# Kernel tuning notes

Hardware: AMD Instinct MI355X
Metric: run time of the kernel (lower is better)

## Reference

```python
import jax, jax.numpy as jnp
import numpy as np

B, T, D = 2, 2048, 2048
H, KV, HD = 16, 8, 128
N_REP = H // KV
EPS = 1e-6
ROPE_THETA = 5e6
K_MASK = float(jnp.finfo(jnp.bfloat16).min)


def setup_inputs() -> dict:
    key = jax.random.key(0)
    ks = jax.random.split(key, 8)
    x = jax.random.normal(ks[0], (B, T, D), dtype=jnp.float32)
    wq = jax.random.normal(ks[1], (D, H * HD), dtype=jnp.float32) * 0.02
    wk = jax.random.normal(ks[2], (D, KV * HD), dtype=jnp.float32) * 0.02
    wv = jax.random.normal(ks[3], (D, KV * HD), dtype=jnp.float32) * 0.02
    wo = jax.random.normal(ks[4], (H * HD, D), dtype=jnp.float32) * 0.02
    qn_w = jnp.ones((HD,), dtype=jnp.float32)
    kn_w = jnp.ones((HD,), dtype=jnp.float32)
    # real rotary angles: [T, HD//2] -> broadcast to [B, T, HD//2]
    pos = jnp.arange(T, dtype=jnp.float32)
    inv_freq = 1.0 / (ROPE_THETA ** (jnp.arange(0, HD, 2, dtype=jnp.float32) / HD))
    ang = pos[:, None] * inv_freq[None, :]
    sin = jnp.broadcast_to(jnp.sin(ang)[None], (B, T, HD // 2))
    cos = jnp.broadcast_to(jnp.cos(ang)[None], (B, T, HD // 2))
    # causal mask [B, 1, T, T]
    causal = jnp.tril(jnp.ones((T, T), dtype=jnp.bool_))
    mask = jnp.broadcast_to(causal[None, None], (B, 1, T, T))
    k_cache = jnp.zeros((B, T, KV, HD), dtype=jnp.float32)
    v_cache = jnp.zeros((B, T, KV, HD), dtype=jnp.float32)
    return {"x": x, "wq": wq, "wk": wk, "wv": wv, "wo": wo,
            "qn_w": qn_w, "kn_w": kn_w, "sin": sin, "cos": cos,
            "mask": mask, "k_cache": k_cache, "v_cache": v_cache}


def _rms_norm(h, w):
    h32 = h.astype(jnp.float32)
    rms = jax.lax.rsqrt(jnp.mean(h32 * h32, axis=-1, keepdims=True) + EPS)
    return (h32 * rms * w).astype(h.dtype)


def _apply_rope(x, sin, cos):
    x1, x2 = x[..., : HD // 2], x[..., HD // 2:]
    s, c = sin[:, :, None, :], cos[:, :, None, :]  # [B,T,1,HD/2]
    return jnp.concatenate([x1 * c - x2 * s, x2 * c + x1 * s], axis=-1).astype(x.dtype)


def reference(x, wq, wk, wv, wo, qn_w, kn_w, sin, cos, mask, k_cache, v_cache):
    b, t, _ = x.shape
    q = _rms_norm((x @ wq).reshape(b, t, H, HD), qn_w)
    k = _rms_norm((x @ wk).reshape(b, t, KV, HD), kn_w)
    v = (x @ wv).reshape(b, t, KV, HD)
    q = _apply_rope(q, sin, cos)
    k = _apply_rope(k, sin, cos)
    # KV-cache update at cur_ind = 0 (prefill)
    k_cache = jax.lax.dynamic_update_slice(k_cache, k.astype(k_cache.dtype), (0, 0, 0, 0))
    v_cache = jax.lax.dynamic_update_slice(v_cache, v.astype(v_cache.dtype), (0, 0, 0, 0))
    # GQA repeat_kv: [B,S,KV,HD] -> [B,S,H,HD]
    kf = jnp.repeat(k_cache, N_REP, axis=2)
    vf = jnp.repeat(v_cache, N_REP, axis=2)
    scale = HD ** -0.5
    # [B,H,T,S]
    attn = jnp.einsum('bthd,bshd->bhts', q, kf) * scale
    attn = jnp.where(mask, attn, K_MASK)
    attn = jax.nn.softmax(attn.astype(jnp.float32), axis=-1).astype(q.dtype)
    out = jnp.einsum('bhts,bshd->bthd', attn, vf).reshape(b, t, H * HD)
    return out @ wo
```

## Files before the change

### kernel.cpp

```cpp
#include <hip/hip_runtime.h>
#include <hip/hip_bf16.h>
#include <stdint.h>

#define BB 2
#define TT 2048
#define DD 2048
#define HH 16
#define KVH 8
#define HDIM 128
#define BT (BB*TT)
#define NQKV (HH*HDIM + 2*KVH*HDIM)
#define TQ (TT/128)
#define ATT_SCALE 0.08838834764831845f
#define RMS_EPS 1e-6f

typedef __bf16 bf16;
typedef __bf16 bf16x8 __attribute__((ext_vector_type(8)));
typedef __bf16 bf16x4 __attribute__((ext_vector_type(4)));
typedef float  f32x4  __attribute__((ext_vector_type(4)));

__device__ __forceinline__ void gl_lds16(const void* g, const void* l) {
  __builtin_amdgcn_global_load_lds(
      (const __attribute__((address_space(1))) void*)(uintptr_t)g,
      (__attribute__((address_space(3))) void*)(uint32_t)(uintptr_t)l,
      16, 0, 0);
}

__global__ __launch_bounds__(256) void cast_bf16_k(const float* __restrict__ in,
                                                   bf16* __restrict__ out, int n4) {
  int i = blockIdx.x * blockDim.x + threadIdx.x;
  int stride = gridDim.x * blockDim.x;
  for (; i < n4; i += stride) {
    float4 v = ((const float4*)in)[i];
    bf16x4 o = { (bf16)v.x, (bf16)v.y, (bf16)v.z, (bf16)v.w };
    *(bf16x4*)(out + (size_t)i * 4) = o;
  }
}

__global__ __launch_bounds__(256) void transpose_cast_k(const float* __restrict__ in,
                                                        bf16* __restrict__ out,
                                                        int R, int C) {
  __shared__ float tile[32][33];
  int tx = threadIdx.x & 31, ty = threadIdx.x >> 5;
  int c0 = blockIdx.x * 32, r0 = blockIdx.y * 32;
#pragma unroll
  for (int i = 0; i < 4; ++i)
    tile[ty + 8*i][tx] = in[(size_t)(r0 + ty + 8*i) * C + c0 + tx];
  __syncthreads();
#pragma unroll
  for (int i = 0; i < 4; ++i)
    out[(size_t)(c0 + ty + 8*i) * R + r0 + tx] = (bf16)tile[tx][ty + 8*i];
}

__global__ __launch_bounds__(256) void transpose_v_k(const bf16* __restrict__ vb,
                                                     bf16* __restrict__ vbt) {
  __shared__ bf16 tile[32][33];
  int tx = threadIdx.x & 31, ty = threadIdx.x >> 5;
  int t0 = blockIdx.x * 32;
  int d0 = blockIdx.y * 32;
  int bk = blockIdx.z;
  int b = bk >> 3, kv = bk & 7;
#pragma unroll
  for (int i = 0; i < 4; ++i)
    tile[ty + 8*i][tx] = vb[(((size_t)(b*TT + t0 + ty + 8*i)) * KVH + kv) * HDIM + d0 + tx];
  __syncthreads();
#pragma unroll
  for (int i = 0; i < 4; ++i)
    vbt[(((size_t)bk) * HDIM + d0 + ty + 8*i) * TT + t0 + tx] = tile[tx][ty + 8*i];
}

template <int OUT_F32>
__global__ __launch_bounds__(512, 2)
void gemm256_k(const bf16* __restrict__ A, const bf16* __restrict__ Bt,
               void* __restrict__ Cout, int M, int N, int K) {
  __shared__ bf16 S[2 * 2 * 2 * 128 * 64];
  const int tid = threadIdx.x, lane = tid & 63, wid = tid >> 6;
  const int lr = lane & 15, lq = lane >> 4;
  const int wrow = wid >> 1, wcol = wid & 1;

  const int nwg = gridDim.x;
  const int o = blockIdx.x;
  const int ns = (o & 7) * (nwg >> 3) + (o >> 3);
  const int GX = N >> 8;
  const int by = ns / GX, bx = ns % GX;

  const int NT = K >> 6;
  const bf16* Ab = A + (size_t)(by * 256) * K;
  const bf16* Bb = Bt + (size_t)(bx * 256) * K;

  const int srow = tid >> 3;
  const size_t soff = (size_t)srow * K + (((tid & 7) ^ (srow & 7)) * 8);
  const int ldst0 = wid * 512;

  auto STAGE = [&](int op, int h, int t_) {
    int tc = t_ < NT ? t_ : NT - 1;
    const bf16* src = (op ? Bb : Ab) + soff + (size_t)(h * 128) * K + tc * 64;
    bf16* dst = S + ((((((t_ & 1) << 1) | op) << 1) | h) << 13) + ldst0;
#pragma unroll
    for (int i = 0; i < 2; ++i)
      gl_lds16(src + (size_t)(i * 64) * K, dst + i * 4096);
  };

  bf16x8 af[2][2][2];
  bf16x8 bfr[4][2];
  f32x4 acc[4][2][4] = {};

  auto LOAD_A = [&](int buf) {
#pragma unroll
    for (int mh = 0; mh < 2; ++mh) {
      const bf16* base = S + (((buf << 2) | mh) << 13);
#pragma unroll
      for (int m = 0; m < 2; ++m) {
        int ra = wrow * 32 + m * 16 + lr;
#pragma unroll
        for (int ks = 0; ks < 2; ++ks)
          af[mh][m][ks] = *(const bf16x8*)(base + ra * 64 + (((ks * 4 + lq) ^ (ra & 7)) * 8));
      }
    }
  };
  auto LOAD_B = [&](int buf, int nh) {
    const bf16* base = S + (((buf << 2) | 2 | nh) << 13);
#pragma unroll
    for (int n = 0; n < 4; ++n) {
      int rb = wcol * 64 + n * 16 + lr;
#pragma unroll
      for (int ks = 0; ks < 2; ++ks)
        bfr[n][ks] = *(const bf16x8*)(base + rb * 64 + (((ks * 4 + lq) ^ (rb & 7)) * 8));
    }
  };
  auto MFMA_Q = [&](int qd, int mh) {
#pragma unroll
    for (int m = 0; m < 2; ++m)
#pragma unroll
      for (int n = 0; n < 4; ++n)
#pragma unroll
        for (int ks = 0; ks < 2; ++ks)
          acc[qd][m][n] = __builtin_amdgcn_mfma_f32_16x16x32_bf16(
              af[mh][m][ks], bfr[n][ks], acc[qd][m][n], 0, 0, 0);
  };

  STAGE(0, 0, 0); STAGE(0, 1, 0); STAGE(1, 0, 0); STAGE(1, 1, 0);
  STAGE(0, 0, 1); STAGE(0, 1, 1); STAGE(1, 0, 1);
  asm volatile("s_waitcnt vmcnt(6)" ::: "memory");
  __builtin_amdgcn_sched_barrier(0);
  __builtin_amdgcn_s_barrier();

  for (int t = 0; t < NT; ++t) {
    const int buf = t & 1;
    LOAD_A(buf);
    LOAD_B(buf, 0);
    STAGE(1, 1, t + 1);
    __builtin_amdgcn_s_barrier();
    asm volatile("s_waitcnt lgkmcnt(0)" ::: "memory");
    __builtin_amdgcn_sched_barrier(0);
    __builtin_amdgcn_s_setprio(1);
    MFMA_Q(0, 0);
    __builtin_amdgcn_s_setprio(0);
    __builtin_amdgcn_sched_barrier(0);
    __builtin_amdgcn_s_barrier();
    STAGE(0, 0, t + 2);
    __builtin_amdgcn_s_barrier();
    __builtin_amdgcn_s_setprio(1);
    MFMA_Q(1, 1);
    __builtin_amdgcn_s_setprio(0);
    __builtin_amdgcn_sched_barrier(0);
    __builtin_amdgcn_s_barrier();
    LOAD_B(buf, 1);
    STAGE(0, 1, t + 2);
    __builtin_amdgcn_s_barrier();
    asm volatile("s_waitcnt lgkmcnt(0)" ::: "memory");
    __builtin_amdgcn_sched_barrier(0);
    __builtin_amdgcn_s_setprio(1);
    MFMA_Q(2, 1);
    __builtin_amdgcn_s_setprio(0);
    __builtin_amdgcn_sched_barrier(0);
    __builtin_amdgcn_s_barrier();
    STAGE(1, 0, t + 2);
    asm volatile("s_waitcnt vmcnt(6)" ::: "memory");
    __builtin_amdgcn_sched_barrier(0);
    __builtin_amdgcn_s_barrier();
    __builtin_amdgcn_s_setprio(1);
    MFMA_Q(3, 0);
    __builtin_amdgcn_s_setprio(0);
    __builtin_amdgcn_sched_barrier(0);
    __builtin_amdgcn_s_barrier();
  }

#pragma unroll
  for (int qd = 0; qd < 4; ++qd) {
    const int mh = (qd == 1 || qd == 2) ? 1 : 0;
    const int nh = (qd >= 2) ? 1 : 0;
#pragma unroll
    for (int m = 0; m < 2; ++m)
#pragma unroll
      for (int n = 0; n < 4; ++n)
#pragma unroll
        for (int j = 0; j < 4; ++j) {
          int row = by * 256 + mh * 128 + wrow * 32 + m * 16 + lq * 4 + j;
          int col = bx * 256 + nh * 128 + wcol * 64 + n * 16 + lr;
          if (OUT_F32) ((float*)Cout)[(size_t)row * N + col] = acc[qd][m][n][j];
          else         ((bf16*)Cout)[(size_t)row * N + col] = (bf16)acc[qd][m][n][j];
        }
  }
}

__global__ __launch_bounds__(256) void norm_rope_k(const bf16* __restrict__ qkv,
                                                   const float* __restrict__ qn_w,
                                                   const float* __restrict__ kn_w,
                                                   const float* __restrict__ sinb,
                                                   const float* __restrict__ cosb,
                                                   bf16* __restrict__ qro,
                                                   bf16* __restrict__ kro,
                                                   bf16* __restrict__ vo) {
  const int bt = blockIdx.x;
  const int tid = threadIdx.x, lane = tid & 63, wid = tid >> 6;
  const bf16* row = qkv + (size_t)bt * NQKV;
  const float sv = sinb[bt * 64 + lane];
  const float cv = cosb[bt * 64 + lane];
  for (int it = 0; it < 8; ++it) {
    int hv = it * 4 + wid;
    int off = (hv < 16) ? hv * 128 : (hv < 24) ? 2048 + (hv - 16) * 128 : 3072 + (hv - 24) * 128;
    float e0 = (float)row[off + lane];
    float e1 = (float)row[off + 64 + lane];
    if (hv >= 24) {
      bf16* dst = vo + (size_t)bt * (KVH * HDIM) + (hv - 24) * 128;
      dst[lane] = (bf16)e0;
      dst[64 + lane] = (bf16)e1;
    } else {
      float ss = e0 * e0 + e1 * e1;
#pragma unroll
      for (int o = 32; o >= 1; o >>= 1) ss += __shfl_xor(ss, o, 64);
      float rms = rsqrtf(ss * (1.0f / 128.0f) + RMS_EPS);
      const float* wn = (hv < 16) ? qn_w : kn_w;
      float n0 = e0 * rms * wn[lane];
      float n1 = e1 * rms * wn[lane + 64];
      float o0 = n0 * cv - n1 * sv;
      float o1 = n1 * cv + n0 * sv;
      if (hv < 16) {
        bf16* dst = qro + (size_t)bt * (HH * HDIM) + hv * 128;
        dst[lane] = (bf16)o0; dst[64 + lane] = (bf16)o1;
      } else {
        bf16* dst = kro + (size_t)bt * (KVH * HDIM) + (hv - 16) * 128;
        dst[lane] = (bf16)o0; dst[64 + lane] = (bf16)o1;
      }
    }
  }
}

__global__ __launch_bounds__(512, 4)
void attn4_k(const bf16* __restrict__ qr, const bf16* __restrict__ kr,
             const bf16* __restrict__ vbt, bf16* __restrict__ ao) {
  __shared__ bf16 Ks[2][64 * 128];
  __shared__ bf16 Vs[2][128 * 64];
  __shared__ bf16 Ps[8 * 16 * 64];
  const int tid = threadIdx.x, lane = tid & 63, wid = tid >> 6;
  const int lr = lane & 15, lq = lane >> 4;
  const int h = blockIdx.y, b = blockIdx.z;
  const int qt = (b & 1) ? (TQ - 1 - blockIdx.x) : blockIdx.x;
  const int kvh = h >> 1;
  const int q0 = qt * 128 + wid * 16;
  const int nt = 2 * qt + 2;

  const int krow0 = lane >> 4, kcc = lane & 15;
  const int vrow0 = lane >> 3, vcc = lane & 7;

  auto STAGE = [&](int bufi, int kt) {
#pragma unroll
    for (int i = 0; i < 2; ++i) {
      int chunk = i * 8 + wid;
      int krow = chunk * 4 + krow0;
      gl_lds16(&kr[(((size_t)(b * TT + kt * 64 + krow)) * KVH + kvh) * HDIM + ((kcc ^ (krow & 7)) * 8)],
               &Ks[bufi][chunk * 512]);
      int drow = chunk * 8 + vrow0;
      gl_lds16(&vbt[(((size_t)(b * KVH + kvh)) * HDIM + drow) * TT + kt * 64 + ((vcc ^ (drow & 7)) * 8)],
               &Vs[bufi][chunk * 512]);
    }
  };

  bf16x8 aq[4];
#pragma unroll
  for (int kk = 0; kk < 4; ++kk)
    aq[kk] = *(const bf16x8*)&qr[(((size_t)(b * TT + q0 + lr)) * HH + h) * HDIM + kk * 32 + lq * 8];

  bf16x8 vones;
#pragma unroll
  for (int j = 0; j < 8; ++j) vones[j] = (bf16)1.0f;

  f32x4 accO[8] = {};
  f32x4 acc1 = {};
  float mrun[4];
#pragma unroll
  for (int r = 0; r < 4; ++r) mrun[r] = -INFINITY;

  int buf = 0;
  STAGE(0, 0);
  __syncthreads();

  for (int kt = 0; kt < nt; ++kt) {
    if (kt + 1 < nt) STAGE(buf ^ 1, kt + 1);

    if (kt * 64 <= q0 + 15) {
      f32x4 sacc[4];
#pragma unroll
      for (int ct = 0; ct < 4; ++ct) {
        sacc[ct] = (f32x4){0.f, 0.f, 0.f, 0.f};
        int krow = ct * 16 + lr;
#pragma unroll
        for (int kk = 0; kk < 4; ++kk) {
          bf16x8 bk = *(const bf16x8*)((const char*)&Ks[buf][0] + krow * 256 + (((kk * 4 + lq) ^ (krow & 7)) * 16));
          sacc[ct] = __builtin_amdgcn_mfma_f32_16x16x32_bf16(aq[kk], bk, sacc[ct], 0, 0, 0);
        }
      }

      const bool domask = (kt * 64 + 63 > q0);
      float p[4][4];
      float pm[4] = {-INFINITY, -INFINITY, -INFINITY, -INFINITY};
#pragma unroll
      for (int ct = 0; ct < 4; ++ct) {
        int col = kt * 64 + ct * 16 + lr;
#pragma unroll
        for (int r = 0; r < 4; ++r) {
          int rowg = q0 + lq * 4 + r;
          float s = (!domask || col <= rowg) ? sacc[ct][r] * ATT_SCALE : -INFINITY;
          p[ct][r] = s;
          pm[r] = fmaxf(pm[r], s);
        }
      }
#pragma unroll
      for (int r = 0; r < 4; ++r) {
#pragma unroll
        for (int o = 1; o < 16; o <<= 1) pm[r] = fmaxf(pm[r], __shfl_xor(pm[r], o, 64));
      }

      int needup = (pm[0] > mrun[0] + 8.f) || (pm[1] > mrun[1] + 8.f) ||
                   (pm[2] > mrun[2] + 8.f) || (pm[3] > mrun[3] + 8.f);
      if (__any(needup)) {
        float alpha[4];
#pragma unroll
        for (int r = 0; r < 4; ++r) {
          float mnew = fmaxf(mrun[r], pm[r]);
          alpha[r] = __expf(mrun[r] - mnew);
          mrun[r] = mnew;
        }
#pragma unroll
        for (int n = 0; n < 8; ++n)
#pragma unroll
          for (int r = 0; r < 4; ++r) accO[n][r] *= alpha[r];
#pragma unroll
        for (int r = 0; r < 4; ++r) acc1[r] *= alpha[r];
      }

#pragma unroll
      for (int ct = 0; ct < 4; ++ct)
#pragma unroll
        for (int r = 0; r < 4; ++r) {
          float e = __expf(p[ct][r] - mrun[r]);
          int prow = lq * 4 + r;
          int col = ct * 16 + lr;
          int cc = col >> 3;
          char* pb = (char*)Ps + (wid * 16 + prow) * 128 + ((cc ^ (prow & 7)) * 16) + (col & 7) * 2;
          *(bf16*)pb = (bf16)e;
        }

#pragma unroll
      for (int c = 0; c < 2; ++c) {
        bf16x8 ap = *(const bf16x8*)((const char*)Ps + (wid * 16 + lr) * 128 + (((c * 4 + lq) ^ (lr & 7)) * 16));
        acc1 = __builtin_amdgcn_mfma_f32_16x16x32_bf16(ap, vones, acc1, 0, 0, 0);
#pragma unroll
        for (int n = 0; n < 8; ++n) {
          int drow = n * 16 + lr;
          bf16x8 bv = *(const bf16x8*)((const char*)&Vs[buf][0] + drow * 128 + (((c * 4 + lq) ^ (drow & 7)) * 16));
          accO[n] = __builtin_amdgcn_mfma_f32_16x16x32_bf16(ap, bv, accO[n], 0, 0, 0);
        }
      }
    }

    __syncthreads();
    buf ^= 1;
  }

  float inv[4];
#pragma unroll
  for (int r = 0; r < 4; ++r) inv[r] = 1.0f / acc1[r];
#pragma unroll
  for (int n = 0; n < 8; ++n)
#pragma unroll
    for (int r = 0; r < 4; ++r) {
      size_t idx = (((size_t)(b * TT + q0 + lq * 4 + r)) * HH + h) * HDIM + n * 16 + lr;
      ao[idx] = (bf16)(accO[n][r] * inv[r]);
    }
}

extern "C" void kernel_launch(void* const* d_in, const int* in_sizes, int n_in,
                              void* d_out, int out_size, void* d_ws, size_t ws_size,
                              hipStream_t stream) {
  const float* x    = (const float*)d_in[0];
  const float* wq   = (const float*)d_in[1];
  const float* wk   = (const float*)d_in[2];
  const float* wv   = (const float*)d_in[3];
  const float* wo   = (const float*)d_in[4];
  const float* qn_w = (const float*)d_in[5];
  const float* kn_w = (const float*)d_in[6];
  const float* sinb = (const float*)d_in[7];
  const float* cosb = (const float*)d_in[8];
  float* out = (float*)d_out;

  char* ws = (char*)d_ws;
  size_t off = 0;
  auto alloc = [&](size_t bytes) {
    char* p = ws + off;
    off += (bytes + 255) & ~(size_t)255;
    return p;
  };
  bf16* xb  = (bf16*)alloc((size_t)BT * DD * 2);
  bf16* Wt  = (bf16*)alloc((size_t)NQKV * DD * 2);
  bf16* Wot = (bf16*)alloc((size_t)DD * DD * 2);
  bf16* qkv = (bf16*)alloc((size_t)BT * NQKV * 2);
  bf16* kro = (bf16*)alloc((size_t)BT * KVH * HDIM * 2);
  bf16* vb  = (bf16*)alloc((size_t)BT * KVH * HDIM * 2);
  bf16* vbt = (bf16*)alloc((size_t)BT * KVH * HDIM * 2);
  bf16* qro = Wt;
  bf16* aob = xb;
  (void)ws_size; (void)in_sizes; (void)n_in; (void)out_size;

  cast_bf16_k<<<2048, 256, 0, stream>>>(x, xb, BT * DD / 4);
  transpose_cast_k<<<dim3(2048 / 32, 2048 / 32), 256, 0, stream>>>(wq, Wt, 2048, 2048);
  transpose_cast_k<<<dim3(1024 / 32, 2048 / 32), 256, 0, stream>>>(wk, Wt + (size_t)2048 * 2048, 2048, 1024);
  transpose_cast_k<<<dim3(1024 / 32, 2048 / 32), 256, 0, stream>>>(wv, Wt + (size_t)3072 * 2048, 2048, 1024);
  transpose_cast_k<<<dim3(2048 / 32, 2048 / 32), 256, 0, stream>>>(wo, Wot, 2048, 2048);

  gemm256_k<0><<<dim3((BT / 256) * (NQKV / 256)), 512, 0, stream>>>(xb, Wt, qkv, BT, NQKV, DD);

  norm_rope_k<<<BT, 256, 0, stream>>>(qkv, qn_w, kn_w, sinb, cosb, qro, kro, vb);
  transpose_v_k<<<dim3(TT / 32, HDIM / 32, BB * KVH), 256, 0, stream>>>(vb, vbt);

  attn4_k<<<dim3(TQ, HH, BB), 512, 0, stream>>>(qro, kro, vbt, aob);

  gemm256_k<1><<<dim3((BT / 256) * (DD / 256)), 512, 0, stream>>>(aob, Wot, out, BT, DD, DD);
}
```

Before: 244.0 us.

## Rewrite attention kernel with 32x32x16 MFMA and register-resident P transposed scores

Replaces the 16x16x32 MFMA attention with a 4-wave block where each wave handles 32 query rows using 32x32x16 bf16 MFMA, computing S transposed (K as A operand) so each lane owns one query column. The probability tile is repacked in registers via cross-half shuffles instead of round-tripping through LDS, and the row sum is accumulated with scalar adds instead of a ones-vector MFMA. This aims to cut LDS traffic and MFMA issue count, but halves threads per block, changes the LDS swizzle, and broadcasts rescale factors through a small shared array with only a waitcnt rather than a barrier.

```diff
diff --git a/kernel.cpp b/kernel.cpp
--- a/kernel.cpp
+++ b/kernel.cpp
@@ -17,13 +17,21 @@
 typedef __bf16 bf16;
 typedef __bf16 bf16x8 __attribute__((ext_vector_type(8)));
 typedef __bf16 bf16x4 __attribute__((ext_vector_type(4)));
+typedef __bf16 bf16x2 __attribute__((ext_vector_type(2)));
 typedef float  f32x4  __attribute__((ext_vector_type(4)));
+typedef float  f32x16 __attribute__((ext_vector_type(16)));
+typedef unsigned u32x4 __attribute__((ext_vector_type(4)));
 
 __device__ __forceinline__ void gl_lds16(const void* g, const void* l) {
   __builtin_amdgcn_global_load_lds(
       (const __attribute__((address_space(1))) void*)(uintptr_t)g,
       (__attribute__((address_space(3))) void*)(uint32_t)(uintptr_t)l,
       16, 0, 0);
+}
+
+__device__ __forceinline__ unsigned pkbf(float lo, float hi) {
+  bf16x2 t = { (bf16)lo, (bf16)hi };
+  return __builtin_bit_cast(unsigned, t);
 }
 
 __global__ __launch_bounds__(256) void cast_bf16_k(const float* __restrict__ in,
@@ -247,50 +255,42 @@
   }
 }
 
-__global__ __launch_bounds__(512, 4)
-void attn4_k(const bf16* __restrict__ qr, const bf16* __restrict__ kr,
+__global__ __launch_bounds__(256, 2)
+void attn5_k(const bf16* __restrict__ qr, const bf16* __restrict__ kr,
              const bf16* __restrict__ vbt, bf16* __restrict__ ao) {
   __shared__ bf16 Ks[2][64 * 128];
   __shared__ bf16 Vs[2][128 * 64];
-  __shared__ bf16 Ps[8 * 16 * 64];
+  __shared__ float Al[4][32];
   const int tid = threadIdx.x, lane = tid & 63, wid = tid >> 6;
-  const int lr = lane & 15, lq = lane >> 4;
+  const int l31 = lane & 31, hi = lane >> 5;
   const int h = blockIdx.y, b = blockIdx.z;
   const int qt = (b & 1) ? (TQ - 1 - blockIdx.x) : blockIdx.x;
   const int kvh = h >> 1;
-  const int q0 = qt * 128 + wid * 16;
+  const int q0w = qt * 128 + wid * 32;
+  const int qg = q0w + l31;
   const int nt = 2 * qt + 2;
 
-  const int krow0 = lane >> 4, kcc = lane & 15;
-  const int vrow0 = lane >> 3, vcc = lane & 7;
-
   auto STAGE = [&](int bufi, int kt) {
 #pragma unroll
-    for (int i = 0; i < 2; ++i) {
-      int chunk = i * 8 + wid;
-      int krow = chunk * 4 + krow0;
-      gl_lds16(&kr[(((size_t)(b * TT + kt * 64 + krow)) * KVH + kvh) * HDIM + ((kcc ^ (krow & 7)) * 8)],
-               &Ks[bufi][chunk * 512]);
-      int drow = chunk * 8 + vrow0;
-      gl_lds16(&vbt[(((size_t)(b * KVH + kvh)) * HDIM + drow) * TT + kt * 64 + ((vcc ^ (drow & 7)) * 8)],
-               &Vs[bufi][chunk * 512]);
-    }
-  };
-
-  bf16x8 aq[4];
-#pragma unroll
-  for (int kk = 0; kk < 4; ++kk)
-    aq[kk] = *(const bf16x8*)&qr[(((size_t)(b * TT + q0 + lr)) * HH + h) * HDIM + kk * 32 + lq * 8];
-
-  bf16x8 vones;
-#pragma unroll
-  for (int j = 0; j < 8; ++j) vones[j] = (bf16)1.0f;
-
-  f32x4 accO[8] = {};
-  f32x4 acc1 = {};
-  float mrun[4];
-#pragma unroll
-  for (int r = 0; r < 4; ++r) mrun[r] = -INFINITY;
+    for (int i = 0; i < 4; ++i) {
+      int u = i * 256 + tid;
+      int krow = u >> 4, kcc = u & 15;
+      gl_lds16(&kr[(((size_t)(b * TT + kt * 64 + krow)) * KVH + kvh) * HDIM + ((kcc ^ (krow & 15)) * 8)],
+               &Ks[bufi][(i * 256 + wid * 64) * 8]);
+      int vrow = u >> 3, vcc = u & 7;
+      gl_lds16(&vbt[(((size_t)(b * KVH + kvh)) * HDIM + vrow) * TT + kt * 64 + ((vcc ^ (vrow & 7)) * 8)],
+               &Vs[bufi][(i * 256 + wid * 64) * 8]);
+    }
+  };
+
+  bf16x8 qf[8];
+  const bf16* qrow = &qr[(((size_t)(b * TT + qg)) * HH + h) * HDIM];
+#pragma unroll
+  for (int ks = 0; ks < 8; ++ks)
+    qf[ks] = *(const bf16x8*)(qrow + ks * 16 + hi * 8);
+
+  f32x16 accO[4] = {};
+  float m = -INFINITY, lsum = 0.f;
 
   int buf = 0;
   STAGE(0, 0);
@@ -299,78 +299,97 @@
   for (int kt = 0; kt < nt; ++kt) {
     if (kt + 1 < nt) STAGE(buf ^ 1, kt + 1);
 
-    if (kt * 64 <= q0 + 15) {
-      f32x4 sacc[4];
-#pragma unroll
-      for (int ct = 0; ct < 4; ++ct) {
-        sacc[ct] = (f32x4){0.f, 0.f, 0.f, 0.f};
-        int krow = ct * 16 + lr;
-#pragma unroll
-        for (int kk = 0; kk < 4; ++kk) {
-          bf16x8 bk = *(const bf16x8*)((const char*)&Ks[buf][0] + krow * 256 + (((kk * 4 + lq) ^ (krow & 7)) * 16));
-          sacc[ct] = __builtin_amdgcn_mfma_f32_16x16x32_bf16(aq[kk], bk, sacc[ct], 0, 0, 0);
-        }
-      }
-
-      const bool domask = (kt * 64 + 63 > q0);
-      float p[4][4];
-      float pm[4] = {-INFINITY, -INFINITY, -INFINITY, -INFINITY};
-#pragma unroll
-      for (int ct = 0; ct < 4; ++ct) {
-        int col = kt * 64 + ct * 16 + lr;
-#pragma unroll
-        for (int r = 0; r < 4; ++r) {
-          int rowg = q0 + lq * 4 + r;
-          float s = (!domask || col <= rowg) ? sacc[ct][r] * ATT_SCALE : -INFINITY;
-          p[ct][r] = s;
-          pm[r] = fmaxf(pm[r], s);
-        }
-      }
-#pragma unroll
-      for (int r = 0; r < 4; ++r) {
-#pragma unroll
-        for (int o = 1; o < 16; o <<= 1) pm[r] = fmaxf(pm[r], __shfl_xor(pm[r], o, 64));
-      }
-
-      int needup = (pm[0] > mrun[0] + 8.f) || (pm[1] > mrun[1] + 8.f) ||
-                   (pm[2] > mrun[2] + 8.f) || (pm[3] > mrun[3] + 8.f);
-      if (__any(needup)) {
-        float alpha[4];
-#pragma unroll
-        for (int r = 0; r < 4; ++r) {
-          float mnew = fmaxf(mrun[r], pm[r]);
-          alpha[r] = __expf(mrun[r] - mnew);
-          mrun[r] = mnew;
-        }
-#pragma unroll
-        for (int n = 0; n < 8; ++n)
-#pragma unroll
-          for (int r = 0; r < 4; ++r) accO[n][r] *= alpha[r];
-#pragma unroll
-        for (int r = 0; r < 4; ++r) acc1[r] *= alpha[r];
-      }
-
-#pragma unroll
-      for (int ct = 0; ct < 4; ++ct)
-#pragma unroll
-        for (int r = 0; r < 4; ++r) {
-          float e = __expf(p[ct][r] - mrun[r]);
-          int prow = lq * 4 + r;
-          int col = ct * 16 + lr;
-          int cc = col >> 3;
-          char* pb = (char*)Ps + (wid * 16 + prow) * 128 + ((cc ^ (prow & 7)) * 16) + (col & 7) * 2;
-          *(bf16*)pb = (bf16)e;
-        }
-
-#pragma unroll
-      for (int c = 0; c < 2; ++c) {
-        bf16x8 ap = *(const bf16x8*)((const char*)Ps + (wid * 16 + lr) * 128 + (((c * 4 + lq) ^ (lr & 7)) * 16));
-        acc1 = __builtin_amdgcn_mfma_f32_16x16x32_bf16(ap, vones, acc1, 0, 0, 0);
-#pragma unroll
-        for (int n = 0; n < 8; ++n) {
-          int drow = n * 16 + lr;
-          bf16x8 bv = *(const bf16x8*)((const char*)&Vs[buf][0] + drow * 128 + (((c * 4 + lq) ^ (drow & 7)) * 16));
-          accO[n] = __builtin_amdgcn_mfma_f32_16x16x32_bf16(ap, bv, accO[n], 0, 0, 0);
+    if (kt * 64 <= q0w + 31) {
+      const char* Kb = (const char*)&Ks[buf][0];
+      const char* Vb = (const char*)&Vs[buf][0];
+
+      f32x16 sacc[2];
+#pragma unroll
+      for (int ct = 0; ct < 2; ++ct) {
+#pragma unroll
+        for (int j = 0; j < 16; ++j) sacc[ct][j] = 0.f;
+        int krow = ct * 32 + l31;
+#pragma unroll
+        for (int ks = 0; ks < 8; ++ks) {
+          bf16x8 kf = *(const bf16x8*)(Kb + krow * 256 + (((2 * ks + hi) ^ (krow & 15)) * 16));
+          sacc[ct] = __builtin_amdgcn_mfma_f32_32x32x16_bf16(kf, qf[ks], sacc[ct], 0, 0, 0);
+        }
+      }
+
+      const bool domask = (kt * 64 + 63 > q0w);
+      float p[2][16];
+      float pmx = -INFINITY;
+#pragma unroll
+      for (int ct = 0; ct < 2; ++ct) {
+        int lim = qg - (kt * 64 + ct * 32 + 4 * hi);
+#pragma unroll
+        for (int r = 0; r < 16; ++r) {
+          const int crow0 = (r & 3) + 8 * (r >> 2);
+          float v = sacc[ct][r] * ATT_SCALE;
+          v = (!domask || crow0 <= lim) ? v : -INFINITY;
+          p[ct][r] = v;
+          pmx = fmaxf(pmx, v);
+        }
+      }
+      pmx = fmaxf(pmx, __shfl_xor(pmx, 32, 64));
+
+      if (__any(pmx > m + 8.f)) {
+        float mnew = fmaxf(m, pmx);
+        float alpha = __expf(m - mnew);
+        m = mnew;
+        lsum *= alpha;
+        if (lane < 32) Al[wid][l31] = alpha;
+        __builtin_amdgcn_s_waitcnt(0);
+#pragma unroll
+        for (int n = 0; n < 4; ++n)
+#pragma unroll
+          for (int r = 0; r < 16; ++r) {
+            const int crow = (r & 3) + 8 * (r >> 2) + 4 * hi;
+            accO[n][r] *= Al[wid][crow];
+          }
+      }
+
+      float rsum = 0.f;
+#pragma unroll
+      for (int ct = 0; ct < 2; ++ct)
+#pragma unroll
+        for (int r = 0; r < 16; ++r) {
+          float e = __expf(p[ct][r] - m);
+          p[ct][r] = e;
+          rsum += e;
+        }
+      rsum += __shfl_xor(rsum, 32, 64);
+      lsum += rsum;
+
+      bf16x8 pa[4];
+#pragma unroll
+      for (int ct = 0; ct < 2; ++ct) {
+        unsigned W[8];
+#pragma unroll
+        for (int mi = 0; mi < 8; ++mi)
+          W[mi] = pkbf(p[ct][2 * mi], p[ct][2 * mi + 1]);
+#pragma unroll
+        for (int a = 0; a < 2; ++a) {
+          unsigned s0 = __shfl_xor(W[4 * a + 0], 32, 64);
+          unsigned s1 = __shfl_xor(W[4 * a + 1], 32, 64);
+          unsigned s2 = __shfl_xor(W[4 * a + 2], 32, 64);
+          unsigned s3 = __shfl_xor(W[4 * a + 3], 32, 64);
+          u32x4 wv;
+          wv[0] = hi ? s2 : W[4 * a + 0];
+          wv[1] = hi ? s3 : W[4 * a + 1];
+          wv[2] = hi ? W[4 * a + 2] : s0;
+          wv[3] = hi ? W[4 * a + 3] : s1;
+          pa[ct * 2 + a] = __builtin_bit_cast(bf16x8, wv);
+        }
+      }
+
+#pragma unroll
+      for (int n = 0; n < 4; ++n) {
+        int vrow = n * 32 + l31;
+#pragma unroll
+        for (int ks = 0; ks < 4; ++ks) {
+          bf16x8 vf = *(const bf16x8*)(Vb + vrow * 128 + (((2 * ks + hi) ^ (vrow & 7)) * 16));
+          accO[n] = __builtin_amdgcn_mfma_f32_32x32x16_bf16(pa[ks], vf, accO[n], 0, 0, 0);
         }
       }
     }
@@ -379,15 +398,17 @@
     buf ^= 1;
   }
 
-  float inv[4];
-#pragma unroll
-  for (int r = 0; r < 4; ++r) inv[r] = 1.0f / acc1[r];
-#pragma unroll
-  for (int n = 0; n < 8; ++n)
-#pragma unroll
-    for (int r = 0; r < 4; ++r) {
-      size_t idx = (((size_t)(b * TT + q0 + lq * 4 + r)) * HH + h) * HDIM + n * 16 + lr;
-      ao[idx] = (bf16)(accO[n][r] * inv[r]);
+  float inv = 1.0f / lsum;
+  __syncthreads();
+  if (lane < 32) Al[wid][l31] = inv;
+  __builtin_amdgcn_s_waitcnt(0);
+#pragma unroll
+  for (int n = 0; n < 4; ++n)
+#pragma unroll
+    for (int r = 0; r < 16; ++r) {
+      const int crow = (r & 3) + 8 * (r >> 2) + 4 * hi;
+      size_t idx = (((size_t)(b * TT + q0w + crow)) * HH + h) * HDIM + n * 32 + l31;
+      ao[idx] = (bf16)(accO[n][r] * Al[wid][crow]);
     }
 }
 
@@ -434,7 +455,7 @@
   norm_rope_k<<<BT, 256, 0, stream>>>(qkv, qn_w, kn_w, sinb, cosb, qro, kro, vb);
   transpose_v_k<<<dim3(TT / 32, HDIM / 32, BB * KVH), 256, 0, stream>>>(vb, vbt);
 
-  attn4_k<<<dim3(TQ, HH, BB), 512, 0, stream>>>(qro, kro, vbt, aob);
+  attn5_k<<<dim3(TQ, HH, BB), 256, 0, stream>>>(qro, kro, vbt, aob);
 
   gemm256_k<1><<<dim3((BT / 256) * (DD / 256)), 512, 0, stream>>>(aob, Wot, out, BT, DD, DD);
 }
```

Result: faster. 231.5 us (-5.1%).
